# Kernel tuning notes

Measured on AMD Instinct MI355X. Metric: run time of the kernel, lower is better.

The kernel has to match this reference:

```python
import jax, jax.numpy as jnp
import numpy as np

B, C, H, W = 8, 512, 64, 64
NUM_HEADS = 8
HEAD_DIM = C // NUM_HEADS
EPS = 1e-5


def setup_inputs() -> dict:
    key = jax.random.key(0)
    k1, k2, k3 = jax.random.split(key, 3)
    x = jax.random.normal(k1, (B, C, H, W), dtype=jnp.float32)
    # xavier-uniform-ish init for 1x1 conv weights (out, in)
    lim_qkv = float(np.sqrt(6.0 / (C + 3 * C)))
    qkv_w = jax.random.uniform(k2, (3 * C, C), dtype=jnp.float32, minval=-lim_qkv, maxval=lim_qkv)
    qkv_b = jnp.zeros((3 * C,), dtype=jnp.float32)
    lim_p = float(np.sqrt(6.0 / (C + C)))
    proj_w = jax.random.uniform(k3, (C, C), dtype=jnp.float32, minval=-lim_p, maxval=lim_p)
    proj_b = jnp.zeros((C,), dtype=jnp.float32)
    return {"x": x, "qkv_w": qkv_w, "qkv_b": qkv_b, "proj_w": proj_w, "proj_b": proj_b}


def _layer_norm_lastdim(x):
    mu = jnp.mean(x, axis=-1, keepdims=True)
    var = jnp.mean(jnp.square(x - mu), axis=-1, keepdims=True)
    return (x - mu) * jax.lax.rsqrt(var + EPS)


def reference(x, qkv_w, qkv_b, proj_w, proj_b):
    b, c, h, w = x.shape
    n = h * w
    nh, hd = NUM_HEADS, c // NUM_HEADS
    # layer norm over channel dim per spatial location (no affine params)
    xt = x.transpose(0, 2, 3, 1).reshape(b, n, c)          # (B, N, C)
    x_norm = _layer_norm_lastdim(xt)
    # qkv 1x1 conv == dense matmul over channels
    qkv = jnp.einsum('bnc,oc->bno', x_norm, qkv_w) + qkv_b  # (B, N, 3C)
    qkv = qkv.reshape(b, n, 3, nh, hd)
    q, k, v = qkv[:, :, 0], qkv[:, :, 1], qkv[:, :, 2]      # each (B, N, nh, hd)
    scale = float(hd) ** -0.5
    # NOTE: torch code contracts over spatial N -> attention matrix is (hd x hd)
    attn = jnp.einsum('bnhi,bnhj->bhij', q, k) * scale      # (B, nh, hd, hd)
    attn = jnp.clip(attn, -50.0, 50.0)
    attn = jax.nn.softmax(attn, axis=-1)
    attn = jnp.where(jnp.isnan(attn), 1.0 / hd, attn)
    out = jnp.einsum('bhij,bnhj->bhin', attn, v)            # (B, nh, hd, N)
    out = out.reshape(b, c, n)                              # (B, C, N)
    out = jnp.einsum('oc,bcn->bon', proj_w, out) + proj_b[None, :, None]
    return out.reshape(b, c, h, w)
```

## Files before the change

### kernel.cpp

```cpp
#include <hip/hip_runtime.h>
#include <cstddef>

#define NBATCH 8
#define NCH 512
#define NTOK 4096
#define NH 8
#define HD 64
#define QKV_M 1536
#define LN_EPS 1e-5f

typedef unsigned short bf16_t;
typedef __attribute__((ext_vector_type(8))) short bf16x8;
typedef __attribute__((ext_vector_type(4))) float f32x4;
typedef __attribute__((ext_vector_type(8))) unsigned short us8;

__device__ __forceinline__ float bf2f(bf16_t u) {
    return __uint_as_float(((unsigned)u) << 16);
}
__device__ __forceinline__ bf16_t f2bf(float f) {
    unsigned u = __float_as_uint(f);
    u += 0x7FFFu + ((u >> 16) & 1u);
    return (bf16_t)(u >> 16);
}

__device__ __forceinline__ void gload_lds16(const void* g, void* l) {
    __builtin_amdgcn_global_load_lds(
        (const __attribute__((address_space(1))) unsigned int*)g,
        (__attribute__((address_space(3))) unsigned int*)l, 16, 0, 0);
}

__global__ __launch_bounds__(256) void ln_stats_kernel(const float* __restrict__ x,
                                                       float* __restrict__ mu,
                                                       float* __restrict__ rr)
{
    int n = blockIdx.x * 256 + threadIdx.x;
    int b = blockIdx.y;
    const float* xb = x + (size_t)b * NCH * NTOK + n;
    float s = 0.f, s2 = 0.f;
    #pragma unroll 8
    for (int c = 0; c < NCH; ++c) {
        float v = xb[(size_t)c * NTOK];
        s += v;
        s2 += v * v;
    }
    float m = s * (1.0f / NCH);
    float var = s2 * (1.0f / NCH) - m * m;
    mu[b * NTOK + n] = m;
    rr[b * NTOK + n] = rsqrtf(var + LN_EPS);
}

__global__ __launch_bounds__(256) void ln_tr_kernel(const float* __restrict__ x,
                                                    const float* __restrict__ mu,
                                                    const float* __restrict__ rr,
                                                    bf16_t* __restrict__ xnt)
{
    int b  = blockIdx.z;
    int n0 = blockIdx.x * 64;
    int c0 = blockIdx.y * 64;
    __shared__ float T[64][65];

    int t = threadIdx.x;
    {
        int cl = t >> 2;
        const float* xr = x + ((size_t)b * NCH + c0 + cl) * NTOK + n0;
        #pragma unroll
        for (int it = 0; it < 4; ++it) {
            int nf = ((t & 3) + it * 4) * 4;
            float4 v = *reinterpret_cast<const float4*>(xr + nf);
            T[cl][nf + 0] = v.x; T[cl][nf + 1] = v.y;
            T[cl][nf + 2] = v.z; T[cl][nf + 3] = v.w;
        }
    }
    __syncthreads();
    int nl = t >> 2;
    int coff = (t & 3) * 16;
    float muv = mu[b * NTOK + n0 + nl];
    float rrv = rr[b * NTOK + n0 + nl];
    us8 o0, o1;
    #pragma unroll
    for (int j = 0; j < 8; ++j) o0[j] = f2bf((T[coff + j][nl] - muv) * rrv);
    #pragma unroll
    for (int j = 0; j < 8; ++j) o1[j] = f2bf((T[coff + 8 + j][nl] - muv) * rrv);
    bf16_t* orow = xnt + ((size_t)b * NTOK + n0 + nl) * NCH + c0 + coff;
    *reinterpret_cast<us8*>(orow)     = o0;
    *reinterpret_cast<us8*>(orow + 8) = o1;
}

__global__ __launch_bounds__(256) void wconv_kernel(const float* __restrict__ w,
                                                    bf16_t* __restrict__ wb)
{
    int i = (blockIdx.x * 256 + threadIdx.x) * 4;
    float4 v = *reinterpret_cast<const float4*>(w + i);
    ushort4 o;
    o.x = f2bf(v.x); o.y = f2bf(v.y); o.z = f2bf(v.z); o.w = f2bf(v.w);
    *reinterpret_cast<ushort4*>(wb + i) = o;
}

__global__ __launch_bounds__(256) void vtr_kernel(const bf16_t* __restrict__ v_tmp,
                                                  bf16_t* __restrict__ vt)
{
    int b  = blockIdx.z;
    int n0 = blockIdx.x * 64;
    int c0 = blockIdx.y * 64;
    __shared__ bf16_t T[64][65];

    int t = threadIdx.x;
    {
        int cl = t >> 2;
        const bf16_t* vr = v_tmp + ((size_t)b * NCH + c0 + cl) * NTOK + n0;
        int nf = (t & 3) * 16;
        us8 a = *reinterpret_cast<const us8*>(vr + nf);
        us8 c = *reinterpret_cast<const us8*>(vr + nf + 8);
        #pragma unroll
        for (int j = 0; j < 8; ++j) { T[cl][nf + j] = a[j]; T[cl][nf + 8 + j] = c[j]; }
    }
    __syncthreads();
    int nl = t >> 2;
    int coff = (t & 3) * 16;
    us8 o0, o1;
    #pragma unroll
    for (int j = 0; j < 8; ++j) o0[j] = T[coff + j][nl];
    #pragma unroll
    for (int j = 0; j < 8; ++j) o1[j] = T[coff + 8 + j][nl];
    bf16_t* orow = vt + ((size_t)b * NTOK + n0 + nl) * NCH + c0 + coff;
    *reinterpret_cast<us8*>(orow)     = o0;
    *reinterpret_cast<us8*>(orow + 8) = o1;
}

template<bool OUT_F32>
__global__ __launch_bounds__(256) void gemm_mfma_kernel(
    const bf16_t* __restrict__ A, size_t sAb,
    const bf16_t* __restrict__ Bt, size_t sBb,
    const float* __restrict__ bias,
    bf16_t* __restrict__ oQK,
    bf16_t* __restrict__ oV,
    float*  __restrict__ oF,
    int M, int K)
{
    int bz = blockIdx.z;
    A  += (size_t)bz * sAb;
    Bt += (size_t)bz * sBb;
    int n0 = blockIdx.x * 128;
    int m0 = blockIdx.y * 128;

    __shared__ __align__(16) bf16_t Als[128 * 64];
    __shared__ __align__(16) bf16_t Bls[128 * 64];

    int tid  = threadIdx.x;
    int wid  = tid >> 6;
    int lane = tid & 63;
    int wr = wid >> 1, wc = wid & 1;
    int lrow = lane & 15;
    int lkg  = lane >> 4;
    int srow = lane >> 3;
    int sc8  = lane & 7;

    f32x4 acc[4][4];
    #pragma unroll
    for (int i = 0; i < 4; ++i)
        #pragma unroll
        for (int j = 0; j < 4; ++j)
            acc[i][j] = (f32x4){0.f, 0.f, 0.f, 0.f};

    for (int k0 = 0; k0 < K; k0 += 64) {
        #pragma unroll
        for (int i = 0; i < 4; ++i) {
            int r = wid * 32 + i * 8 + srow;
            int koff = k0 + ((sc8 ^ (r & 7)) << 3);
            gload_lds16(A  + (size_t)(m0 + r) * K + koff, Als + (wid * 32 + i * 8) * 64);
            gload_lds16(Bt + (size_t)(n0 + r) * K + koff, Bls + (wid * 32 + i * 8) * 64);
        }
        __syncthreads();
        #pragma unroll
        for (int ks = 0; ks < 2; ++ks) {
            int kg = ks * 4 + lkg;
            bf16x8 af[4], bfv[4];
            #pragma unroll
            for (int i = 0; i < 4; ++i) {
                int row = wr * 64 + i * 16 + lrow;
                af[i] = *reinterpret_cast<const bf16x8*>(Als + row * 64 + ((kg ^ (row & 7)) << 3));
            }
            #pragma unroll
            for (int j = 0; j < 4; ++j) {
                int row = wc * 64 + j * 16 + lrow;
                bfv[j] = *reinterpret_cast<const bf16x8*>(Bls + row * 64 + ((kg ^ (row & 7)) << 3));
            }
            #pragma unroll
            for (int i = 0; i < 4; ++i)
                #pragma unroll
                for (int j = 0; j < 4; ++j)
                    acc[i][j] = __builtin_amdgcn_mfma_f32_16x16x32_bf16(af[i], bfv[j], acc[i][j], 0, 0, 0);
        }
        __syncthreads();
    }

    #pragma unroll
    for (int i = 0; i < 4; ++i) {
        #pragma unroll
        for (int r = 0; r < 4; ++r) {
            int m = m0 + wr * 64 + i * 16 + (lane >> 4) * 4 + r;
            float bv = bias[m];
            #pragma unroll
            for (int j = 0; j < 4; ++j) {
                int n = n0 + wc * 64 + j * 16 + (lane & 15);
                float v = acc[i][j][r] + bv;
                if (OUT_F32) {
                    oF[((size_t)bz * M + m) * NTOK + n] = v;
                } else {
                    bf16_t ob = f2bf(v);
                    if (m0 < 1024) oQK[((size_t)bz * 1024 + m) * NTOK + n] = ob;
                    else           oV[((size_t)bz * NCH + (m - 1024)) * NTOK + n] = ob;
                }
            }
        }
    }
}

__global__ __launch_bounds__(256) void qk_kernel(const bf16_t* __restrict__ qk_buf,
                                                 float* __restrict__ attn_part)
{
    int chunk = blockIdx.x;
    int bh = blockIdx.y;
    int b = bh >> 3, h = bh & 7;
    const bf16_t* Q  = qk_buf + ((size_t)b * 1024 + h * HD) * NTOK + chunk * 512;
    const bf16_t* Kp = Q + (size_t)NCH * NTOK;

    __shared__ float Qs[64][65];
    __shared__ float Ks[64][65];

    int tid = threadIdx.x;
    int ti = tid >> 4;
    int tj = tid & 15;

    float acc[4][4];
    #pragma unroll
    for (int i = 0; i < 4; ++i)
        #pragma unroll
        for (int j = 0; j < 4; ++j) acc[i][j] = 0.f;

    int lr = tid >> 4;
    int lc = (tid & 15) * 4;

    for (int cc = 0; cc < 512; cc += 64) {
        __syncthreads();
        #pragma unroll
        for (int r = 0; r < 64; r += 16) {
            ushort4 qv = *reinterpret_cast<const ushort4*>(&Q[(size_t)(lr + r) * NTOK + cc + lc]);
            ushort4 kv = *reinterpret_cast<const ushort4*>(&Kp[(size_t)(lr + r) * NTOK + cc + lc]);
            Qs[lr + r][lc + 0] = bf2f(qv.x); Qs[lr + r][lc + 1] = bf2f(qv.y);
            Qs[lr + r][lc + 2] = bf2f(qv.z); Qs[lr + r][lc + 3] = bf2f(qv.w);
            Ks[lr + r][lc + 0] = bf2f(kv.x); Ks[lr + r][lc + 1] = bf2f(kv.y);
            Ks[lr + r][lc + 2] = bf2f(kv.z); Ks[lr + r][lc + 3] = bf2f(kv.w);
        }
        __syncthreads();
        #pragma unroll 4
        for (int kk = 0; kk < 64; ++kk) {
            float qv[4], kv[4];
            #pragma unroll
            for (int i2 = 0; i2 < 4; ++i2) qv[i2] = Qs[ti * 4 + i2][kk];
            #pragma unroll
            for (int j2 = 0; j2 < 4; ++j2) kv[j2] = Ks[tj * 4 + j2][kk];
            #pragma unroll
            for (int i2 = 0; i2 < 4; ++i2)
                #pragma unroll
                for (int j2 = 0; j2 < 4; ++j2)
                    acc[i2][j2] += qv[i2] * kv[j2];
        }
    }
    #pragma unroll
    for (int i2 = 0; i2 < 4; ++i2)
        #pragma unroll
        for (int j2 = 0; j2 < 4; ++j2)
            attn_part[(((size_t)chunk * 64 + bh) * 64 + ti * 4 + i2) * 64 + tj * 4 + j2] = acc[i2][j2];
}

__global__ __launch_bounds__(256) void softmax_kernel(const float* __restrict__ attn_part,
                                                      float* __restrict__ attn)
{
    int bh = blockIdx.x;
    int wave = threadIdx.x >> 6;
    int lane = threadIdx.x & 63;
    for (int i = wave; i < 64; i += 4) {
        float s = 0.f;
        #pragma unroll
        for (int p = 0; p < 8; ++p)
            s += attn_part[(((size_t)p * 64 + bh) * 64 + i) * 64 + lane];
        s *= 0.125f;
        s = fminf(fmaxf(s, -50.f), 50.f);
        float m = s;
        #pragma unroll
        for (int off = 32; off > 0; off >>= 1) m = fmaxf(m, __shfl_xor(m, off, 64));
        float e = __expf(s - m);
        float sum = e;
        #pragma unroll
        for (int off = 32; off > 0; off >>= 1) sum += __shfl_xor(sum, off, 64);
        float p = e / sum;
        if (p != p) p = 1.0f / HD;
        attn[((size_t)bh * 64 + i) * 64 + lane] = p;
    }
}

__global__ __launch_bounds__(256) void fold_kernel(const float* __restrict__ Pw,
                                                   const float* __restrict__ attn,
                                                   bf16_t* __restrict__ wfold)
{
    int bh = blockIdx.y;
    int b = bh >> 3, h = bh & 7;
    int o0 = blockIdx.x * 64;

    __shared__ float Ps[64][68];
    __shared__ float Am[64][68];

    int tid = threadIdx.x;
    {
        int r  = tid >> 2;
        int cq = (tid & 3) * 4;
        #pragma unroll
        for (int j = 0; j < 4; ++j) {
            int c = cq + j * 16;
            *reinterpret_cast<float4*>(&Ps[r][c]) =
                *reinterpret_cast<const float4*>(&Pw[(size_t)(o0 + r) * NCH + h * HD + c]);
            *reinterpret_cast<float4*>(&Am[r][c]) =
                *reinterpret_cast<const float4*>(&attn[((size_t)bh * 64 + r) * 64 + c]);
        }
    }
    __syncthreads();

    int to = tid >> 4;
    int tj = tid & 15;
    float acc[4][4];
    #pragma unroll
    for (int i = 0; i < 4; ++i)
        #pragma unroll
        for (int j = 0; j < 4; ++j) acc[i][j] = 0.f;

    for (int i = 0; i < 64; ++i) {
        float pv[4];
        #pragma unroll
        for (int ii = 0; ii < 4; ++ii) pv[ii] = Ps[to * 4 + ii][i];
        float4 av = *reinterpret_cast<const float4*>(&Am[i][tj * 4]);
        float avr[4] = {av.x, av.y, av.z, av.w};
        #pragma unroll
        for (int ii = 0; ii < 4; ++ii)
            #pragma unroll
            for (int jj = 0; jj < 4; ++jj)
                acc[ii][jj] += pv[ii] * avr[jj];
    }

    #pragma unroll
    for (int ii = 0; ii < 4; ++ii)
        #pragma unroll
        for (int jj = 0; jj < 4; ++jj)
            wfold[((size_t)b * NCH + o0 + to * 4 + ii) * NCH + h * HD + tj * 4 + jj] = f2bf(acc[ii][jj]);
}

extern "C" void kernel_launch(void* const* d_in, const int* in_sizes, int n_in,
                              void* d_out, int out_size, void* d_ws, size_t ws_size,
                              hipStream_t stream)
{
    const float* x      = (const float*)d_in[0];
    const float* qkv_w  = (const float*)d_in[1];
    const float* qkv_b  = (const float*)d_in[2];
    const float* proj_w = (const float*)d_in[3];
    const float* proj_b = (const float*)d_in[4];
    float* out = (float*)d_out;

    float* mu        = (float*)d_ws;
    float* rr        = mu + 32768;
    float* attn_part = rr + 32768;
    float* attn      = attn_part + 2097152;
    bf16_t* wfold    = (bf16_t*)(attn + 262144);
    bf16_t* w_bf     = wfold + 2097152;
    bf16_t* qk_buf   = w_bf + 786432;
    bf16_t* vt       = qk_buf + (size_t)33554432;

    bf16_t* xnt   = (bf16_t*)d_out;
    bf16_t* v_tmp = (bf16_t*)d_out + 16777216;

    ln_stats_kernel<<<dim3(NTOK / 256, NBATCH), 256, 0, stream>>>(x, mu, rr);

    ln_tr_kernel<<<dim3(NTOK / 64, NCH / 64, NBATCH), 256, 0, stream>>>(x, mu, rr, xnt);

    wconv_kernel<<<dim3(QKV_M * NCH / 1024), 256, 0, stream>>>(qkv_w, w_bf);

    gemm_mfma_kernel<false><<<dim3(NTOK / 128, QKV_M / 128, NBATCH), 256, 0, stream>>>(
        w_bf, 0, xnt, (size_t)NTOK * NCH, qkv_b, qk_buf, v_tmp, nullptr, QKV_M, NCH);

    vtr_kernel<<<dim3(NTOK / 64, NCH / 64, NBATCH), 256, 0, stream>>>(v_tmp, vt);

    qk_kernel<<<dim3(8, 64), 256, 0, stream>>>(qk_buf, attn_part);

    softmax_kernel<<<64, 256, 0, stream>>>(attn_part, attn);

    fold_kernel<<<dim3(8, 64), 256, 0, stream>>>(proj_w, attn, wfold);

    gemm_mfma_kernel<true><<<dim3(NTOK / 128, NCH / 128, NBATCH), 256, 0, stream>>>(
        wfold, (size_t)NCH * NCH, vt, (size_t)NTOK * NCH, proj_b,
        nullptr, nullptr, out, NCH, NCH);
}
```

Measured before the change: 346.5 us.

## Compute V transposed directly via swapped GEMM and use MFMA for QK

The V projection now runs as a separate GEMM with operands swapped (xnt as A, V weights as B) so its output lands directly in token-major layout, removing the separate V transpose kernel and its round trip through memory. The GEMM kernel gains a column-bias mode and a generic leading dimension. The fp32 LDS-tiled Q·K^T reduction is replaced by an MFMA bf16 kernel that reads fragments straight from global memory. This adds one GEMM launch in place of the transpose, and the QK kernel's uncached strided global loads may limit how much it helps.

```diff
diff --git a/kernel.cpp b/kernel.cpp
--- a/kernel.cpp
+++ b/kernel.cpp
@@ -96,46 +96,14 @@
     *reinterpret_cast<ushort4*>(wb + i) = o;
 }
 
-__global__ __launch_bounds__(256) void vtr_kernel(const bf16_t* __restrict__ v_tmp,
-                                                  bf16_t* __restrict__ vt)
-{
-    int b  = blockIdx.z;
-    int n0 = blockIdx.x * 64;
-    int c0 = blockIdx.y * 64;
-    __shared__ bf16_t T[64][65];
-
-    int t = threadIdx.x;
-    {
-        int cl = t >> 2;
-        const bf16_t* vr = v_tmp + ((size_t)b * NCH + c0 + cl) * NTOK + n0;
-        int nf = (t & 3) * 16;
-        us8 a = *reinterpret_cast<const us8*>(vr + nf);
-        us8 c = *reinterpret_cast<const us8*>(vr + nf + 8);
-        #pragma unroll
-        for (int j = 0; j < 8; ++j) { T[cl][nf + j] = a[j]; T[cl][nf + 8 + j] = c[j]; }
-    }
-    __syncthreads();
-    int nl = t >> 2;
-    int coff = (t & 3) * 16;
-    us8 o0, o1;
-    #pragma unroll
-    for (int j = 0; j < 8; ++j) o0[j] = T[coff + j][nl];
-    #pragma unroll
-    for (int j = 0; j < 8; ++j) o1[j] = T[coff + 8 + j][nl];
-    bf16_t* orow = vt + ((size_t)b * NTOK + n0 + nl) * NCH + c0 + coff;
-    *reinterpret_cast<us8*>(orow)     = o0;
-    *reinterpret_cast<us8*>(orow + 8) = o1;
-}
-
-template<bool OUT_F32>
+template<bool OUT_F32, bool BIAS_COL>
 __global__ __launch_bounds__(256) void gemm_mfma_kernel(
     const bf16_t* __restrict__ A, size_t sAb,
     const bf16_t* __restrict__ Bt, size_t sBb,
     const float* __restrict__ bias,
-    bf16_t* __restrict__ oQK,
-    bf16_t* __restrict__ oV,
-    float*  __restrict__ oF,
-    int M, int K)
+    bf16_t* __restrict__ ob,
+    float*  __restrict__ of,
+    int ldC, int M, int K)
 {
     int bz = blockIdx.z;
     A  += (size_t)bz * sAb;
@@ -199,79 +167,57 @@
         #pragma unroll
         for (int r = 0; r < 4; ++r) {
             int m = m0 + wr * 64 + i * 16 + (lane >> 4) * 4 + r;
-            float bv = bias[m];
+            float bvr = BIAS_COL ? 0.f : bias[m];
             #pragma unroll
             for (int j = 0; j < 4; ++j) {
                 int n = n0 + wc * 64 + j * 16 + (lane & 15);
-                float v = acc[i][j][r] + bv;
-                if (OUT_F32) {
-                    oF[((size_t)bz * M + m) * NTOK + n] = v;
-                } else {
-                    bf16_t ob = f2bf(v);
-                    if (m0 < 1024) oQK[((size_t)bz * 1024 + m) * NTOK + n] = ob;
-                    else           oV[((size_t)bz * NCH + (m - 1024)) * NTOK + n] = ob;
-                }
+                float v = acc[i][j][r] + (BIAS_COL ? bias[n] : bvr);
+                if (OUT_F32) of[((size_t)bz * M + m) * ldC + n] = v;
+                else         ob[((size_t)bz * M + m) * ldC + n] = f2bf(v);
             }
         }
     }
 }
 
-__global__ __launch_bounds__(256) void qk_kernel(const bf16_t* __restrict__ qk_buf,
-                                                 float* __restrict__ attn_part)
+__global__ __launch_bounds__(256) void qk_mfma_kernel(const bf16_t* __restrict__ qk_buf,
+                                                      float* __restrict__ attn_part)
 {
     int chunk = blockIdx.x;
     int bh = blockIdx.y;
     int b = bh >> 3, h = bh & 7;
-    const bf16_t* Q  = qk_buf + ((size_t)b * 1024 + h * HD) * NTOK + chunk * 512;
+    const bf16_t* Q  = qk_buf + ((size_t)b * 1024 + h * HD) * NTOK;
     const bf16_t* Kp = Q + (size_t)NCH * NTOK;
 
-    __shared__ float Qs[64][65];
-    __shared__ float Ks[64][65];
-
     int tid = threadIdx.x;
-    int ti = tid >> 4;
-    int tj = tid & 15;
-
-    float acc[4][4];
-    #pragma unroll
-    for (int i = 0; i < 4; ++i)
-        #pragma unroll
-        for (int j = 0; j < 4; ++j) acc[i][j] = 0.f;
-
-    int lr = tid >> 4;
-    int lc = (tid & 15) * 4;
-
-    for (int cc = 0; cc < 512; cc += 64) {
-        __syncthreads();
-        #pragma unroll
-        for (int r = 0; r < 64; r += 16) {
-            ushort4 qv = *reinterpret_cast<const ushort4*>(&Q[(size_t)(lr + r) * NTOK + cc + lc]);
-            ushort4 kv = *reinterpret_cast<const ushort4*>(&Kp[(size_t)(lr + r) * NTOK + cc + lc]);
-            Qs[lr + r][lc + 0] = bf2f(qv.x); Qs[lr + r][lc + 1] = bf2f(qv.y);
-            Qs[lr + r][lc + 2] = bf2f(qv.z); Qs[lr + r][lc + 3] = bf2f(qv.w);
-            Ks[lr + r][lc + 0] = bf2f(kv.x); Ks[lr + r][lc + 1] = bf2f(kv.y);
-            Ks[lr + r][lc + 2] = bf2f(kv.z); Ks[lr + r][lc + 3] = bf2f(kv.w);
-        }
-        __syncthreads();
-        #pragma unroll 4
-        for (int kk = 0; kk < 64; ++kk) {
-            float qv[4], kv[4];
-            #pragma unroll
-            for (int i2 = 0; i2 < 4; ++i2) qv[i2] = Qs[ti * 4 + i2][kk];
-            #pragma unroll
-            for (int j2 = 0; j2 < 4; ++j2) kv[j2] = Ks[tj * 4 + j2][kk];
-            #pragma unroll
-            for (int i2 = 0; i2 < 4; ++i2)
-                #pragma unroll
-                for (int j2 = 0; j2 < 4; ++j2)
-                    acc[i2][j2] += qv[i2] * kv[j2];
-        }
-    }
-    #pragma unroll
-    for (int i2 = 0; i2 < 4; ++i2)
-        #pragma unroll
-        for (int j2 = 0; j2 < 4; ++j2)
-            attn_part[(((size_t)chunk * 64 + bh) * 64 + ti * 4 + i2) * 64 + tj * 4 + j2] = acc[i2][j2];
+    int w = tid >> 6;
+    int lane = tid & 63;
+    int frow = lane & 15;
+    int kg = lane >> 4;
+
+    f32x4 acc[4];
+    #pragma unroll
+    for (int j = 0; j < 4; ++j) acc[j] = (f32x4){0.f, 0.f, 0.f, 0.f};
+
+    const bf16_t* Qrow = Q + (size_t)(w * 16 + frow) * NTOK + chunk * 512 + kg * 8;
+    const bf16_t* Krow = Kp + (size_t)frow * NTOK + chunk * 512 + kg * 8;
+
+    for (int ks = 0; ks < 16; ++ks) {
+        bf16x8 af = *reinterpret_cast<const bf16x8*>(Qrow + ks * 32);
+        #pragma unroll
+        for (int j = 0; j < 4; ++j) {
+            bf16x8 bfv = *reinterpret_cast<const bf16x8*>(Krow + (size_t)(j * 16) * NTOK + ks * 32);
+            acc[j] = __builtin_amdgcn_mfma_f32_16x16x32_bf16(af, bfv, acc[j], 0, 0, 0);
+        }
+    }
+
+    #pragma unroll
+    for (int j = 0; j < 4; ++j)
+        #pragma unroll
+        for (int r = 0; r < 4; ++r) {
+            int i  = w * 16 + (lane >> 4) * 4 + r;
+            int jj = j * 16 + (lane & 15);
+            attn_part[(((size_t)chunk * 64 + bh) * 64 + i) * 64 + jj] = acc[j][r];
+        }
 }
 
 __global__ __launch_bounds__(256) void softmax_kernel(const float* __restrict__ attn_part,
@@ -374,8 +320,7 @@
     bf16_t* qk_buf   = w_bf + 786432;
     bf16_t* vt       = qk_buf + (size_t)33554432;
 
-    bf16_t* xnt   = (bf16_t*)d_out;
-    bf16_t* v_tmp = (bf16_t*)d_out + 16777216;
+    bf16_t* xnt = (bf16_t*)d_out;
 
     ln_stats_kernel<<<dim3(NTOK / 256, NBATCH), 256, 0, stream>>>(x, mu, rr);
 
@@ -383,18 +328,20 @@
 
     wconv_kernel<<<dim3(QKV_M * NCH / 1024), 256, 0, stream>>>(qkv_w, w_bf);
 
-    gemm_mfma_kernel<false><<<dim3(NTOK / 128, QKV_M / 128, NBATCH), 256, 0, stream>>>(
-        w_bf, 0, xnt, (size_t)NTOK * NCH, qkv_b, qk_buf, v_tmp, nullptr, QKV_M, NCH);
-
-    vtr_kernel<<<dim3(NTOK / 64, NCH / 64, NBATCH), 256, 0, stream>>>(v_tmp, vt);
-
-    qk_kernel<<<dim3(8, 64), 256, 0, stream>>>(qk_buf, attn_part);
+    gemm_mfma_kernel<false, false><<<dim3(NTOK / 128, 1024 / 128, NBATCH), 256, 0, stream>>>(
+        w_bf, 0, xnt, (size_t)NTOK * NCH, qkv_b, qk_buf, nullptr, NTOK, 1024, NCH);
+
+    gemm_mfma_kernel<false, true><<<dim3(NCH / 128, NTOK / 128, NBATCH), 256, 0, stream>>>(
+        xnt, (size_t)NTOK * NCH, w_bf + (size_t)1024 * NCH, 0, qkv_b + 1024,
+        vt, nullptr, NCH, NTOK, NCH);
+
+    qk_mfma_kernel<<<dim3(8, 64), 256, 0, stream>>>(qk_buf, attn_part);
 
     softmax_kernel<<<64, 256, 0, stream>>>(attn_part, attn);
 
     fold_kernel<<<dim3(8, 64), 256, 0, stream>>>(proj_w, attn, wfold);
 
-    gemm_mfma_kernel<true><<<dim3(NTOK / 128, NCH / 128, NBATCH), 256, 0, stream>>>(
+    gemm_mfma_kernel<true, false><<<dim3(NTOK / 128, NCH / 128, NBATCH), 256, 0, stream>>>(
         wfold, (size_t)NCH * NCH, vt, (size_t)NTOK * NCH, proj_b,
-        nullptr, nullptr, out, NCH, NCH);
-}
+        nullptr, out, NTOK, NCH, NCH);
+}
```

New measurement: 313.2 us. -9.6%, faster.
